# Kernel tuning notes

Hardware: AMD Instinct MI355X
Metric: run time of the kernel (lower is better)

## Reference

```python
import jax, jax.numpy as jnp
import numpy as np
import math

B, L, D, H = 4, 2048, 512, 8
DH = D // H
FACTOR = 5.0
EPS = 1e-9
# static top-k count: min(L_q, max(1, int(factor * log(L_q + eps))))
K_TOP = min(L, max(1, int(FACTOR * math.log(L + EPS))))  # = 38
SCALE = 1.0 / math.sqrt(DH)


def setup_inputs() -> dict:
    key = jax.random.key(0)
    ks = jax.random.split(key, 9)
    s = 1.0 / math.sqrt(D)
    return {
        "x": jax.random.normal(ks[0], (B, L, D), jnp.float32),
        "Wq": jax.random.normal(ks[1], (D, D), jnp.float32) * s,
        "bq": jax.random.normal(ks[2], (D,), jnp.float32) * 0.01,
        "Wk": jax.random.normal(ks[3], (D, D), jnp.float32) * s,
        "bk": jax.random.normal(ks[4], (D,), jnp.float32) * 0.01,
        "Wv": jax.random.normal(ks[5], (D, D), jnp.float32) * s,
        "bv": jax.random.normal(ks[6], (D,), jnp.float32) * 0.01,
        "Wo": jax.random.normal(ks[7], (D, D), jnp.float32) * s,
        "bo": jax.random.normal(ks[8], (D,), jnp.float32) * 0.01,
    }


def _project(x, W, b):
    # [B, L, D] -> [B*H, L, DH]
    y = x @ W + b
    return y.reshape(B, L, H, DH).transpose(0, 2, 1, 3).reshape(B * H, L, DH)


def reference(x, Wq, bq, Wk, bk, Wv, bv, Wo, bo):
    Q = _project(x, Wq, bq)
    K = _project(x, Wk, bk)
    V = _project(x, Wv, bv)

    # full scores for sparsity measure: [BH, L, L]
    scores = jnp.einsum('bqd,bkd->bqk', Q, K) * SCALE
    M = scores.max(axis=-1) - scores.mean(axis=-1)  # [BH, L]
    _, top_idx = jax.lax.top_k(M, K_TOP)            # [BH, K_TOP]

    # gather sparse queries, sparse attention
    Q_sparse = jnp.take_along_axis(Q, top_idx[:, :, None], axis=1)  # [BH, K_TOP, DH]
    scores_sparse = jnp.einsum('bqd,bkd->bqk', Q_sparse, K) * SCALE
    attn = jax.nn.softmax(scores_sparse, axis=-1)
    context_sparse = attn @ V                                        # [BH, K_TOP, DH]

    # mean-filled context, scatter sparse results back
    V_mean = V.mean(axis=1, keepdims=True)                           # [BH, 1, DH]
    context = jnp.broadcast_to(V_mean, (B * H, L, DH))
    bidx = jnp.arange(B * H)[:, None]
    context = context.at[bidx, top_idx, :].set(context_sparse)

    # merge heads, output projection
    out = context.reshape(B, H, L, DH).transpose(0, 2, 1, 3).reshape(B, L, D)
    return out @ Wo + bo
```

## Files before the change

### kernel.cpp

```cpp
#include <hip/hip_runtime.h>

#define BB   4
#define LL   2048
#define DD   512
#define HH   8
#define DH   64
#define BH   32
#define KTOP 38
#define NCAND 64
#define SCALEF 0.125f

#define NSP  16
#define CHK  128
#define QPAD 48
#define SCS  132
#define VST  66

typedef __attribute__((ext_vector_type(8))) short bf16x8;
typedef __attribute__((ext_vector_type(8))) unsigned short ushort8;
typedef __attribute__((ext_vector_type(4))) float f32x4;

__device__ __forceinline__ ushort f32_to_bf16_rn(float x) {
    unsigned u = __float_as_uint(x);
    u += 0x7fffu + ((u >> 16) & 1u);
    return (ushort)(u >> 16);
}
__device__ __forceinline__ float bf16_to_f32(ushort h) {
    return __uint_as_float(((unsigned)h) << 16);
}
__device__ __forceinline__ unsigned int pack_hl(float x) {
    ushort h = f32_to_bf16_rn(x);
    ushort l = f32_to_bf16_rn(x - bf16_to_f32(h));
    return ((unsigned int)l << 16) | (unsigned int)h;
}

__global__ __launch_bounds__(256) void split_x(const float* __restrict__ X,
                                               ushort* __restrict__ XH,
                                               ushort* __restrict__ XL) {
    const size_t c = (size_t)blockIdx.x * 256 + threadIdx.x;
    const float4 v = *(const float4*)&X[c * 4];
    ushort4 h, l;
    h.x = f32_to_bf16_rn(v.x); l.x = f32_to_bf16_rn(v.x - bf16_to_f32(h.x));
    h.y = f32_to_bf16_rn(v.y); l.y = f32_to_bf16_rn(v.y - bf16_to_f32(h.y));
    h.z = f32_to_bf16_rn(v.z); l.z = f32_to_bf16_rn(v.z - bf16_to_f32(h.z));
    h.w = f32_to_bf16_rn(v.w); l.w = f32_to_bf16_rn(v.w - bf16_to_f32(h.w));
    *(ushort4*)&XH[c * 4] = h;
    *(ushort4*)&XL[c * 4] = l;
}

__global__ __launch_bounds__(256) void split_wT(const float* __restrict__ W0,
                                                const float* __restrict__ W1,
                                                const float* __restrict__ W2,
                                                ushort* __restrict__ WTH,
                                                ushort* __restrict__ WTL) {
    __shared__ float tile[32][33];
    const int z = blockIdx.z;
    const float* W = (z == 0) ? W0 : (z == 1) ? W1 : W2;
    ushort* oh = WTH + (size_t)z * DD * DD;
    ushort* ol = WTL + (size_t)z * DD * DD;
    const int n0 = blockIdx.x * 32, k0 = blockIdx.y * 32;
    const int t = threadIdx.x;
    const int r = t >> 5, c = t & 31;
    #pragma unroll
    for (int i = 0; i < 4; i++)
        tile[r + i * 8][c] = W[(size_t)(k0 + r + i * 8) * DD + n0 + c];
    __syncthreads();
    #pragma unroll
    for (int i = 0; i < 4; i++) {
        int row = r + i * 8;
        float v = tile[c][row];
        ushort h = f32_to_bf16_rn(v);
        oh[(size_t)(n0 + row) * DD + k0 + c] = h;
        ol[(size_t)(n0 + row) * DD + k0 + c] = f32_to_bf16_rn(v - bf16_to_f32(h));
    }
}

__global__ __launch_bounds__(256) void mfma_gemm_qkv(const ushort* __restrict__ AH,
                                                     const ushort* __restrict__ AL,
                                                     const ushort* __restrict__ BTH,
                                                     const ushort* __restrict__ BTL,
                                                     const float* __restrict__ bq,
                                                     const float* __restrict__ bk,
                                                     const float* __restrict__ bv,
                                                     float* __restrict__ Qp,
                                                     float* __restrict__ Kp,
                                                     float* __restrict__ Vp,
                                                     ushort* __restrict__ KH) {
    __shared__ ushort BHs[64 * 72];
    __shared__ ushort BLs[64 * 72];

    const int t = threadIdx.x;
    const int w = t >> 6, lane = t & 63;
    const int quad = lane >> 4, n16 = lane & 15;
    const int row0 = blockIdx.y * 128;
    const int n0   = blockIdx.x * 64;
    const int z    = n0 >> 9;
    const int nloc0 = n0 & 511;

    const float* bias = (z == 0) ? bq : (z == 1) ? bk : bv;
    float* Y          = (z == 0) ? Qp : (z == 1) ? Kp : Vp;

    f32x4 acc[2][4] = {};

    size_t arow_off[2];
    #pragma unroll
    for (int mt = 0; mt < 2; mt++)
        arow_off[mt] = (size_t)(row0 + w * 32 + mt * 16 + n16) * DD;

    const size_t bbase = (size_t)z * DD * DD;

    for (int k0 = 0; k0 < DD; k0 += 64) {
        #pragma unroll
        for (int i = 0; i < 2; i++) {
            int s = i * 256 + t;
            int row = s >> 3, c8 = s & 7;
            const size_t goff = bbase + (size_t)(nloc0 + row) * DD + k0 + c8 * 8;
            *(uint4*)&BHs[row * 72 + c8 * 8] = *(const uint4*)&BTH[goff];
            *(uint4*)&BLs[row * 72 + c8 * 8] = *(const uint4*)&BTL[goff];
        }
        bf16x8 ah[2][2], al[2][2];
        #pragma unroll
        for (int mt = 0; mt < 2; mt++)
            #pragma unroll
            for (int kf = 0; kf < 2; kf++) {
                size_t off = arow_off[mt] + k0 + kf * 32 + quad * 8;
                ah[mt][kf] = *(const bf16x8*)&AH[off];
                al[mt][kf] = *(const bf16x8*)&AL[off];
            }
        __syncthreads();

        #pragma unroll
        for (int kf = 0; kf < 2; kf++)
            #pragma unroll
            for (int nt = 0; nt < 4; nt++) {
                int boff = (nt * 16 + n16) * 72 + kf * 32 + quad * 8;
                bf16x8 bh = *(const bf16x8*)&BHs[boff];
                bf16x8 bl = *(const bf16x8*)&BLs[boff];
                #pragma unroll
                for (int mt = 0; mt < 2; mt++) {
                    acc[mt][nt] = __builtin_amdgcn_mfma_f32_16x16x32_bf16(ah[mt][kf], bh, acc[mt][nt], 0, 0, 0);
                    acc[mt][nt] = __builtin_amdgcn_mfma_f32_16x16x32_bf16(ah[mt][kf], bl, acc[mt][nt], 0, 0, 0);
                    acc[mt][nt] = __builtin_amdgcn_mfma_f32_16x16x32_bf16(al[mt][kf], bh, acc[mt][nt], 0, 0, 0);
                }
            }
        __syncthreads();
    }

    #pragma unroll
    for (int mt = 0; mt < 2; mt++)
        #pragma unroll
        for (int nt = 0; nt < 4; nt++) {
            const int c = nloc0 + nt * 16 + n16;
            const float bvv = bias[c];
            const int h = c >> 6, dh = c & 63;
            #pragma unroll
            for (int r = 0; r < 4; r++) {
                int R = row0 + w * 32 + mt * 16 + quad * 4 + r;
                int b = R >> 11, l = R & 2047;
                float v = acc[mt][nt][r] + bvv;
                size_t off = (((size_t)(b * HH + h)) * LL + l) * DH + dh;
                Y[off] = v;
                if (z == 1) KH[off] = f32_to_bf16_rn(v);
            }
        }
}

__global__ __launch_bounds__(256) void mean_partial(const float* __restrict__ Kp,
                                                    const float* __restrict__ Vp,
                                                    float* __restrict__ partial) {
    __shared__ float red[256];
    const int bh = blockIdx.x;
    const int srcI = blockIdx.y;
    const int z  = blockIdx.z;
    const float* src = srcI ? Vp : Kp;
    const int t = threadIdx.x;
    const int d = t & 63, ch = t >> 6;
    const int l0 = z * 128 + ch * 32;
    float s = 0.f;
    for (int l = l0; l < l0 + 32; l++)
        s += src[((size_t)bh * LL + l) * DH + d];
    red[t] = s;
    __syncthreads();
    if (t < 64)
        partial[((size_t)((bh * 2 + srcI) * 16 + z)) * 64 + t] =
            red[t] + red[t + 64] + red[t + 128] + red[t + 192];
}

__global__ __launch_bounds__(64) void mean_reduce(const float* __restrict__ partial,
                                                  float* __restrict__ Kmean,
                                                  float* __restrict__ Vmean) {
    const int bh = blockIdx.x;
    const int srcI = blockIdx.y;
    const int t  = threadIdx.x;
    float s = 0.f;
    #pragma unroll
    for (int z = 0; z < 16; z++)
        s += partial[((size_t)((bh * 2 + srcI) * 16 + z)) * 64 + t];
    float* dst = srcI ? Vmean : Kmean;
    dst[bh * DH + t] = s * (1.0f / LL);
}

__global__ __launch_bounds__(256) void base_kernel(const float* __restrict__ Vmean,
                                                   const float* __restrict__ Wo,
                                                   const float* __restrict__ bo,
                                                   float* __restrict__ BASE) {
    __shared__ float vm[512];
    const int b = blockIdx.x;
    const int t = threadIdx.x;
    vm[t]       = Vmean[b * 512 + t];
    vm[t + 256] = Vmean[b * 512 + t + 256];
    __syncthreads();
    #pragma unroll
    for (int cc = 0; cc < 2; cc++) {
        const int c = cc * 256 + t;
        float s = 0.f;
        for (int k = 0; k < 512; k++) s += vm[k] * Wo[(size_t)k * 512 + c];
        BASE[b * 512 + c] = s + bo[c];
    }
}

__global__ __launch_bounds__(256) void broadcast_base(const float* __restrict__ BASE,
                                                      float* __restrict__ out) {
    const size_t f = ((size_t)blockIdx.x * 256 + threadIdx.x) * 4;
    const int b = (int)(f >> 20);
    const int c = (int)(f & 511);
    *(float4*)&out[f] = *(const float4*)&BASE[b * 512 + c];
}

__global__ __launch_bounds__(256) void scatter_kernel(const float* __restrict__ CORR,
                                                      const int* __restrict__ TIDX,
                                                      const float* __restrict__ Wo,
                                                      float* __restrict__ out) {
    __shared__ float cr[64];
    const int q = blockIdx.x, bh = blockIdx.y;
    const int b = bh >> 3, h = bh & 7;
    const int t = threadIdx.x;
    if (t < 64) cr[t] = CORR[((size_t)bh * KTOP + q) * DH + t];
    __syncthreads();
    const int l = TIDX[bh * KTOP + q];
    #pragma unroll
    for (int cc = 0; cc < 2; cc++) {
        const int c = cc * 256 + t;
        float s = 0.f;
        #pragma unroll
        for (int d = 0; d < 64; d++) s += cr[d] * Wo[(size_t)(h * 64 + d) * 512 + c];
        atomicAdd(&out[((size_t)b * LL + l) * DD + c], s);
    }
}

__global__ __launch_bounds__(256) void mfma_stats(const float* __restrict__ Qp,
                                                  const ushort* __restrict__ KH,
                                                  const float* __restrict__ Kmean,
                                                  float* __restrict__ MP,
                                                  float* __restrict__ MMD) {
    __shared__ ushort KS[128 * 72];
    __shared__ float  Km[64];

    const int bh = blockIdx.y;
    const int q0 = blockIdx.x * 128;
    const int z  = blockIdx.z;
    const int t    = threadIdx.x;
    const int w    = t >> 6;
    const int lane = t & 63;
    const int quad = lane >> 4;
    const int n16  = lane & 15;

    if (z == 0) {
        if (t < 64) Km[t] = Kmean[bh * DH + t];
        __syncthreads();
        if (t < 128) {
            const float4* qr = (const float4*)&Qp[((size_t)bh * LL + q0 + t) * DH];
            const float4* km4 = (const float4*)Km;
            float md = 0.f;
            #pragma unroll
            for (int i = 0; i < 16; i++) {
                float4 a = qr[i], b = km4[i];
                md += a.x * b.x + a.y * b.y + a.z * b.z + a.w * b.w;
            }
            MMD[(size_t)bh * LL + q0 + t] = SCALEF * md;
        }
    }

    bf16x8 aH[2][2], aL[2][2];
    #pragma unroll
    for (int mt = 0; mt < 2; mt++) {
        const float* qrp = &Qp[((size_t)bh * LL + q0 + w * 32 + mt * 16 + n16) * DH + quad * 8];
        float v[16];
        *(float4*)&v[0]  = *(const float4*)(qrp);
        *(float4*)&v[4]  = *(const float4*)(qrp + 4);
        *(float4*)&v[8]  = *(const float4*)(qrp + 32);
        *(float4*)&v[12] = *(const float4*)(qrp + 36);
        #pragma unroll
        for (int j = 0; j < 8; j++) {
            ushort h0 = f32_to_bf16_rn(v[j]);
            aH[mt][0][j] = (short)h0;
            aL[mt][0][j] = (short)f32_to_bf16_rn(v[j] - bf16_to_f32(h0));
            ushort h1 = f32_to_bf16_rn(v[8 + j]);
            aH[mt][1][j] = (short)h1;
            aL[mt][1][j] = (short)f32_to_bf16_rn(v[8 + j] - bf16_to_f32(h1));
        }
    }

    f32x4 maxv[2] = {{-3.4e38f, -3.4e38f, -3.4e38f, -3.4e38f},
                     {-3.4e38f, -3.4e38f, -3.4e38f, -3.4e38f}};

    const int kbase = z * (LL / 2);
    for (int kt0 = kbase; kt0 < kbase + LL / 2; kt0 += 128) {
        __syncthreads();
        #pragma unroll
        for (int i = 0; i < 4; i++) {
            int f = i * 256 + t;
            int row = f >> 3, c8 = f & 7;
            const uint4 v = *(const uint4*)&KH[((size_t)(bh * LL + kt0 + row)) * DH + c8 * 8];
            *(uint4*)&KS[row * 72 + c8 * 8] = v;
        }
        __syncthreads();

        for (int ktl = 0; ktl < 128; ktl += 16) {
            const ushort* bp = &KS[(size_t)(ktl + n16) * 72 + quad * 8];
            bf16x8 bH0 = *(const bf16x8*)(bp);
            bf16x8 bH1 = *(const bf16x8*)(bp + 32);
            #pragma unroll
            for (int mt = 0; mt < 2; mt++) {
                f32x4 acc = {0.f, 0.f, 0.f, 0.f};
                acc = __builtin_amdgcn_mfma_f32_16x16x32_bf16(aH[mt][0], bH0, acc, 0, 0, 0);
                acc = __builtin_amdgcn_mfma_f32_16x16x32_bf16(aH[mt][1], bH1, acc, 0, 0, 0);
                acc = __builtin_amdgcn_mfma_f32_16x16x32_bf16(aL[mt][0], bH0, acc, 0, 0, 0);
                acc = __builtin_amdgcn_mfma_f32_16x16x32_bf16(aL[mt][1], bH1, acc, 0, 0, 0);
                maxv[mt][0] = fmaxf(maxv[mt][0], acc[0]);
                maxv[mt][1] = fmaxf(maxv[mt][1], acc[1]);
                maxv[mt][2] = fmaxf(maxv[mt][2], acc[2]);
                maxv[mt][3] = fmaxf(maxv[mt][3], acc[3]);
            }
        }
    }

    #pragma unroll
    for (int off = 1; off < 16; off <<= 1)
        #pragma unroll
        for (int mt = 0; mt < 2; mt++)
            #pragma unroll
            for (int r = 0; r < 4; r++)
                maxv[mt][r] = fmaxf(maxv[mt][r], __shfl_xor(maxv[mt][r], off));

    if (n16 == 0) {
        #pragma unroll
        for (int mt = 0; mt < 2; mt++)
            #pragma unroll
            for (int r = 0; r < 4; r++) {
                int lq = w * 32 + mt * 16 + quad * 4 + r;
                MP[((size_t)z * BH + bh) * LL + q0 + lq] = SCALEF * maxv[mt][r];
            }
    }
}

__global__ __launch_bounds__(256) void topk_radix(const float* __restrict__ MP,
                                                  const float* __restrict__ MMD,
                                                  int* __restrict__ out_idx) {
    __shared__ unsigned hist[4096];
    __shared__ unsigned segc[256];
    __shared__ unsigned suf[256];
    __shared__ int sb1, sc1, sb2;
    __shared__ int ncnt;
    const int bh = blockIdx.x;
    const int t  = threadIdx.x;

    unsigned key[8];
    #pragma unroll
    for (int i = 0; i < 8; i++) {
        size_t q = (size_t)i * 256 + t;
        float v = fmaxf(MP[(size_t)bh * LL + q], MP[((size_t)BH + bh) * LL + q])
                  - MMD[(size_t)bh * LL + q];
        unsigned u = __float_as_uint(v);
        key[i] = (u & 0x80000000u) ? ~u : (u | 0x80000000u);
    }

    #pragma unroll
    for (int i = 0; i < 16; i++) hist[t * 16 + i] = 0;
    if (t == 0) ncnt = 0;
    __syncthreads();
    #pragma unroll
    for (int i = 0; i < 8; i++) atomicAdd(&hist[key[i] >> 20], 1u);
    __syncthreads();
    unsigned s = 0;
    #pragma unroll
    for (int i = 0; i < 16; i++) s += hist[t * 16 + i];
    segc[t] = s;
    __syncthreads();
    if (t == 0) {
        unsigned run = 0;
        for (int i = 255; i >= 0; i--) { suf[i] = run; run += segc[i]; }
    }
    __syncthreads();
    if (suf[t] < NCAND && suf[t] + segc[t] >= NCAND) {
        unsigned c = suf[t];
        for (int j = 15; j >= 0; j--) {
            int b = t * 16 + j;
            if (c + hist[b] >= NCAND) { sb1 = b; sc1 = (int)c; break; }
            c += hist[b];
        }
    }
    __syncthreads();
    const unsigned b1 = (unsigned)sb1;
    const int c1 = sc1;

    #pragma unroll
    for (int i = 0; i < 16; i++) hist[t * 16 + i] = 0;
    __syncthreads();
    #pragma unroll
    for (int i = 0; i < 8; i++)
        if ((key[i] >> 20) == b1) atomicAdd(&hist[(key[i] >> 8) & 0xfffu], 1u);
    __syncthreads();
    s = 0;
    #pragma unroll
    for (int i = 0; i < 16; i++) s += hist[t * 16 + i];
    segc[t] = s;
    __syncthreads();
    if (t == 0) {
        unsigned run = 0;
        for (int i = 255; i >= 0; i--) { suf[i] = run; run += segc[i]; }
    }
    __syncthreads();
    const int need2 = NCAND - c1;
    if ((int)suf[t] < need2 && (int)(suf[t] + segc[t]) >= need2) {
        unsigned c = suf[t];
        for (int j = 15; j >= 0; j--) {
            int b = t * 16 + j;
            if ((int)(c + hist[b]) >= need2) { sb2 = b; break; }
            c += hist[b];
        }
    }
    __syncthreads();
    const unsigned b2 = (unsigned)sb2;

    #pragma unroll
    for (int i = 0; i < 8; i++)
        if ((key[i] >> 20) > b1) {
            int p = atomicAdd(&ncnt, 1);
            out_idx[bh * NCAND + p] = i * 256 + t;
        }
    __syncthreads();
    #pragma unroll
    for (int i = 0; i < 8; i++)
        if ((key[i] >> 20) == b1 && ((key[i] >> 8) & 0xfffu) > b2) {
            int p = atomicAdd(&ncnt, 1);
            out_idx[bh * NCAND + p] = i * 256 + t;
        }
    __syncthreads();
    #pragma unroll
    for (int i = 0; i < 8; i++)
        if ((key[i] >> 20) == b1 && ((key[i] >> 8) & 0xfffu) == b2) {
            int p = atomicAdd(&ncnt, 1);
            if (p < NCAND) out_idx[bh * NCAND + p] = i * 256 + t;
        }
}

__global__ __launch_bounds__(256) void exact_partial(const float* __restrict__ Qp,
                                                     const float* __restrict__ Kp,
                                                     const int* __restrict__ CAND,
                                                     float* __restrict__ EMP) {
    __shared__ float Qs[64][65];
    __shared__ float Ks[64][65];
    __shared__ int   cidx[64];
    const int bh = blockIdx.y;
    const int chunk = blockIdx.x;
    const int t = threadIdx.x;
    const int tx = t & 15, ty = t >> 4;

    if (t < 64) cidx[t] = CAND[bh * NCAND + t];
    __syncthreads();
    #pragma unroll
    for (int i = 0; i < 4; i++) {
        int f = i * 256 + t;
        int row = f >> 4, c4 = f & 15;
        const float4 v = *(const float4*)&Qp[((size_t)bh * LL + cidx[row]) * DH + c4 * 4];
        *(float4*)&Qs[row][c4 * 4] = v;
    }

    float mx[4] = {-3.4e38f, -3.4e38f, -3.4e38f, -3.4e38f};

    for (int kt = 0; kt < 4; kt++) {
        __syncthreads();
        #pragma unroll
        for (int i = 0; i < 4; i++) {
            int f = i * 256 + t;
            int row = f >> 4, c4 = f & 15;
            const float4 v = *(const float4*)&Kp[((size_t)(bh * LL + chunk * 256 + kt * 64 + row)) * DH + c4 * 4];
            *(float4*)&Ks[row][c4 * 4] = v;
        }
        __syncthreads();
        float acc[4][4] = {};
        #pragma unroll 8
        for (int dd = 0; dd < 64; dd++) {
            float a[4], b[4];
            #pragma unroll
            for (int i = 0; i < 4; i++) a[i] = Qs[ty * 4 + i][dd];
            #pragma unroll
            for (int j = 0; j < 4; j++) b[j] = Ks[tx * 4 + j][dd];
            #pragma unroll
            for (int i = 0; i < 4; i++)
                #pragma unroll
                for (int j = 0; j < 4; j++) acc[i][j] += a[i] * b[j];
        }
        #pragma unroll
        for (int i = 0; i < 4; i++)
            #pragma unroll
            for (int j = 0; j < 4; j++) mx[i] = fmaxf(mx[i], acc[i][j]);
    }

    #pragma unroll
    for (int off = 1; off < 16; off <<= 1)
        #pragma unroll
        for (int i = 0; i < 4; i++)
            mx[i] = fmaxf(mx[i], __shfl_xor(mx[i], off));

    if (tx == 0) {
        #pragma unroll
        for (int i = 0; i < 4; i++)
            EMP[((size_t)bh * NCAND + ty * 4 + i) * 8 + chunk] = mx[i];
    }
}

__global__ __launch_bounds__(64) void select_kernel(const float* __restrict__ EMP,
                                                    const int* __restrict__ CAND,
                                                    const float* __restrict__ Qp,
                                                    const float* __restrict__ Kmean,
                                                    int* __restrict__ TIDX) {
    __shared__ float Km[64];
    const int bh = blockIdx.x;
    const int t  = threadIdx.x;
    Km[t] = Kmean[bh * DH + t];
    __syncthreads();

    const int qi = CAND[bh * NCAND + t];
    float mx = -3.4e38f;
    #pragma unroll
    for (int c = 0; c < 8; c++) mx = fmaxf(mx, EMP[((size_t)bh * NCAND + t) * 8 + c]);

    const float4* qr = (const float4*)&Qp[((size_t)bh * LL + qi) * DH];
    const float4* km4 = (const float4*)Km;
    float md = 0.f;
    #pragma unroll
    for (int i = 0; i < 16; i++) {
        float4 a = qr[i], b = km4[i];
        md += a.x * b.x + a.y * b.y + a.z * b.z + a.w * b.w;
    }
    float v = SCALEF * mx - SCALEF * md;

    for (int it = 0; it < KTOP; it++) {
        float bv = v; int bq = qi;
        #pragma unroll
        for (int off = 1; off < 64; off <<= 1) {
            float ov = __shfl_xor(bv, off);
            int   oq = __shfl_xor(bq, off);
            if (ov > bv || (ov == bv && oq < bq)) { bv = ov; bq = oq; }
        }
        if (t == 0) TIDX[bh * KTOP + it] = bq;
        if (qi == bq) v = -3.4e38f;
    }
}

__global__ __launch_bounds__(256) void sparse_partial(const float* __restrict__ Qp,
                                                      const ushort* __restrict__ KH,
                                                      const float* __restrict__ Vp,
                                                      const int* __restrict__ TIDX,
                                                      float* __restrict__ OPART,
                                                      float* __restrict__ MPART,
                                                      float* __restrict__ LPART) {
    __shared__ float sc[QPAD * SCS];
    __shared__ unsigned int Vhl[CHK * VST];
    const int bh = blockIdx.y;
    const int ck = blockIdx.x;
    const int k0 = ck * CHK;
    const int t = threadIdx.x;
    const int w = t >> 6, lane = t & 63;
    const int quad = lane >> 4, n16 = lane & 15;
    const int mt = w;

    #pragma unroll
    for (int i = 0; i < 8; i++) {
        int e = i * 256 + t;
        int key = e >> 4, c4 = e & 15;
        const float4 v = *(const float4*)&Vp[((size_t)(bh * LL + k0 + key)) * DH + c4 * 4];
        uint4 p;
        p.x = pack_hl(v.x); p.y = pack_hl(v.y);
        p.z = pack_hl(v.z); p.w = pack_hl(v.w);
        *(uint4*)&Vhl[key * VST + c4 * 4] = p;
    }

    if (mt < 3) {
        bf16x8 aH[2], aL[2];
        {
            int q = mt * 16 + n16;
            int qq = q < KTOP ? q : (KTOP - 1);
            const float* qp = &Qp[((size_t)bh * LL + TIDX[bh * KTOP + qq]) * DH];
            #pragma unroll
            for (int kf = 0; kf < 2; kf++) {
                float v[8];
                *(float4*)&v[0] = *(const float4*)(qp + kf * 32 + quad * 8);
                *(float4*)&v[4] = *(const float4*)(qp + kf * 32 + quad * 8 + 4);
                #pragma unroll
                for (int j = 0; j < 8; j++) {
                    ushort h = f32_to_bf16_rn(v[j]);
                    aH[kf][j] = (short)h;
                    aL[kf][j] = (short)f32_to_bf16_rn(v[j] - bf16_to_f32(h));
                }
            }
        }
        #pragma unroll
        for (int nt = 0; nt < 8; nt++) {
            f32x4 acc = {0.f, 0.f, 0.f, 0.f};
            #pragma unroll
            for (int kf = 0; kf < 2; kf++) {
                bf16x8 b = *(const bf16x8*)&KH[((size_t)(bh * LL + k0 + nt * 16 + n16)) * DH + kf * 32 + quad * 8];
                acc = __builtin_amdgcn_mfma_f32_16x16x32_bf16(aH[kf], b, acc, 0, 0, 0);
                acc = __builtin_amdgcn_mfma_f32_16x16x32_bf16(aL[kf], b, acc, 0, 0, 0);
            }
            #pragma unroll
            for (int r = 0; r < 4; r++)
                sc[(mt * 16 + quad * 4 + r) * SCS + nt * 16 + n16] = acc[r];
        }
    }
    __syncthreads();

    for (int row = w; row < KTOP; row += 4) {
        float v0 = sc[row * SCS + lane];
        float v1 = sc[row * SCS + 64 + lane];
        float m = fmaxf(v0, v1);
        #pragma unroll
        for (int off = 1; off < 64; off <<= 1)
            m = fmaxf(m, __shfl_xor(m, off));
        const float ms = m * SCALEF;
        float e0 = __expf(v0 * SCALEF - ms);
        float e1 = __expf(v1 * SCALEF - ms);
        float l = e0 + e1;
        #pragma unroll
        for (int off = 1; off < 64; off <<= 1)
            l += __shfl_xor(l, off);
        sc[row * SCS + lane]      = e0;
        sc[row * SCS + 64 + lane] = e1;
        if (lane == 0) {
            MPART[((size_t)ck * BH + bh) * KTOP + row] = ms;
            LPART[((size_t)ck * BH + bh) * KTOP + row] = l;
        }
    }
    __syncthreads();

    if (mt < 3) {
        f32x4 acc[4] = {};
        #pragma unroll
        for (int kf = 0; kf < 4; kf++) {
            bf16x8 ph, pl;
            {
                const float* pp = &sc[(mt * 16 + n16) * SCS + kf * 32 + quad * 8];
                float v[8];
                *(float4*)&v[0] = *(const float4*)(pp);
                *(float4*)&v[4] = *(const float4*)(pp + 4);
                #pragma unroll
                for (int j = 0; j < 8; j++) {
                    ushort h = f32_to_bf16_rn(v[j]);
                    ph[j] = (short)h;
                    pl[j] = (short)f32_to_bf16_rn(v[j] - bf16_to_f32(h));
                }
            }
            #pragma unroll
            for (int nt = 0; nt < 4; nt++) {
                unsigned int u[8];
                #pragma unroll
                for (int j = 0; j < 8; j++)
                    u[j] = Vhl[(kf * 32 + quad * 8 + j) * VST + nt * 16 + n16];
                bf16x8 vh, vl;
                #pragma unroll
                for (int j = 0; j < 8; j++) {
                    vh[j] = (short)(u[j] & 0xffffu);
                    vl[j] = (short)(u[j] >> 16);
                }
                acc[nt] = __builtin_amdgcn_mfma_f32_16x16x32_bf16(ph, vh, acc[nt], 0, 0, 0);
                acc[nt] = __builtin_amdgcn_mfma_f32_16x16x32_bf16(ph, vl, acc[nt], 0, 0, 0);
                acc[nt] = __builtin_amdgcn_mfma_f32_16x16x32_bf16(pl, vh, acc[nt], 0, 0, 0);
            }
        }
        #pragma unroll
        for (int nt = 0; nt < 4; nt++)
            #pragma unroll
            for (int r = 0; r < 4; r++) {
                int q = mt * 16 + quad * 4 + r;
                if (q < KTOP)
                    OPART[(((size_t)ck * BH + bh) * KTOP + q) * DH + nt * 16 + n16] = acc[nt][r];
            }
    }
}

__global__ __launch_bounds__(256) void sparse_combine(const float* __restrict__ OPART,
                                                      const float* __restrict__ MPART,
                                                      const float* __restrict__ LPART,
                                                      const float* __restrict__ Vmean,
                                                      float* __restrict__ CORR) {
    __shared__ float wts[NSP][KTOP];
    __shared__ float inv[KTOP];
    const int bh = blockIdx.x;
    const int t  = threadIdx.x;
    if (t < KTOP) {
        float m[NSP];
        float mx = -3.4e38f;
        #pragma unroll
        for (int c = 0; c < NSP; c++) {
            m[c] = MPART[((size_t)c * BH + bh) * KTOP + t];
            mx = fmaxf(mx, m[c]);
        }
        float L = 0.f;
        #pragma unroll
        for (int c = 0; c < NSP; c++) {
            float wc = __expf(m[c] - mx);
            wts[c][t] = wc;
            L += wc * LPART[((size_t)c * BH + bh) * KTOP + t];
        }
        inv[t] = 1.0f / L;
    }
    __syncthreads();
    for (int i = 0; i < 10; i++) {
        int idx = i * 256 + t;
        if (idx >= KTOP * DH) break;
        int q = idx >> 6, d = idx & 63;
        float o = 0.f;
        #pragma unroll
        for (int c = 0; c < NSP; c++)
            o += wts[c][q] * OPART[(((size_t)c * BH + bh) * KTOP + q) * DH + d];
        CORR[((size_t)bh * KTOP + q) * DH + d] = o * inv[q] - Vmean[bh * DH + d];
    }
}

extern "C" void kernel_launch(void* const* d_in, const int* in_sizes, int n_in,
                              void* d_out, int out_size, void* d_ws, size_t ws_size,
                              hipStream_t stream) {
    const float* x  = (const float*)d_in[0];
    const float* Wq = (const float*)d_in[1];
    const float* bq = (const float*)d_in[2];
    const float* Wk = (const float*)d_in[3];
    const float* bk = (const float*)d_in[4];
    const float* Wv = (const float*)d_in[5];
    const float* bv = (const float*)d_in[6];
    const float* Wo = (const float*)d_in[7];
    const float* bo = (const float*)d_in[8];
    float* out = (float*)d_out;

    float* ws = (float*)d_ws;
    const size_t QSZ = (size_t)BH * LL * DH;
    float* Qp    = ws;
    float* Kp    = ws + QSZ;
    float* Vp    = ws + 2 * QSZ;
    float* MMD   = ws + 3 * QSZ;
    float* KMEAN = MMD + (size_t)BH * LL;
    float* VMEAN = KMEAN + BH * DH;
    int*   CAND  = (int*)(VMEAN + BH * DH);
    int*   TIDX  = CAND + BH * NCAND;
    float* EMP   = (float*)(TIDX + BH * KTOP);
    float* MEANP = EMP + (size_t)BH * NCAND * 8;
    float* MP    = MEANP + 65536;
    float* CORR  = MP + (size_t)2 * BH * LL;
    float* BASE  = CORR + (size_t)BH * KTOP * DH;
    ushort* WTH  = (ushort*)(ws + 3 * QSZ + 786432);
    ushort* WTL  = WTH + (size_t)3 * DD * DD;
    ushort* XH   = WTL + (size_t)3 * DD * DD;
    ushort* XL   = XH + QSZ;
    ushort* KH   = XL + QSZ;
    float* OPART = (float*)(KH + QSZ);
    float* MPART = OPART + (size_t)NSP * BH * KTOP * DH;
    float* LPART = MPART + (size_t)NSP * BH * KTOP;

    split_wT<<<dim3(16, 16, 3), 256, 0, stream>>>(Wq, Wk, Wv, WTH, WTL);
    split_x<<<(int)(QSZ / 1024), 256, 0, stream>>>(x, XH, XL);

    mfma_gemm_qkv<<<dim3(24, 64), 256, 0, stream>>>(XH, XL, WTH, WTL,
                                                    bq, bk, bv, Qp, Kp, Vp, KH);

    mean_partial<<<dim3(BH, 2, 16), 256, 0, stream>>>(Kp, Vp, MEANP);
    mean_reduce<<<dim3(BH, 2), 64, 0, stream>>>(MEANP, KMEAN, VMEAN);

    base_kernel<<<BB, 256, 0, stream>>>(VMEAN, Wo, bo, BASE);
    broadcast_base<<<(int)(QSZ / 1024), 256, 0, stream>>>(BASE, out);

    mfma_stats<<<dim3(16, BH, 2), 256, 0, stream>>>(Qp, KH, KMEAN, MP, MMD);

    topk_radix<<<BH, 256, 0, stream>>>(MP, MMD, CAND);

    exact_partial<<<dim3(8, BH), 256, 0, stream>>>(Qp, Kp, CAND, EMP);

    select_kernel<<<BH, 64, 0, stream>>>(EMP, CAND, Qp, KMEAN, TIDX);

    sparse_partial<<<dim3(NSP, BH), 256, 0, stream>>>(Qp, KH, Vp, TIDX, OPART, MPART, LPART);
    sparse_combine<<<BH, 256, 0, stream>>>(OPART, MPART, LPART, VMEAN, CORR);

    scatter_kernel<<<dim3(KTOP, BH), 256, 0, stream>>>(CORR, TIDX, Wo, out);
}
```

Before: 312.1 us.

## Register-prefetch next tiles in QKV GEMM and stats; fold combine into scatter

The QKV projection GEMM and the stats kernel now prefetch the next k-tile (weights, activations, or K rows) into registers while MFMAs run on the current LDS tile. This hides global-load latency behind compute, at the cost of extra registers. The separate sparse_combine kernel is removed and its softmax-partial merge runs inside scatter_kernel. That saves one launch and the CORR round trip through memory, but each scatter block now recomputes the merge for its own query.

```diff
diff --git a/kernel.cpp b/kernel.cpp
--- a/kernel.cpp
+++ b/kernel.cpp
@@ -108,26 +108,54 @@
         arow_off[mt] = (size_t)(row0 + w * 32 + mt * 16 + n16) * DD;
 
     const size_t bbase = (size_t)z * DD * DD;
-
-    for (int k0 = 0; k0 < DD; k0 += 64) {
+    const int srow = t >> 3, sc8 = t & 7;
+
+    uint4 bregH[2], bregL[2];
+    #pragma unroll
+    for (int i = 0; i < 2; i++) {
+        const int row = srow + i * 32;
+        const size_t goff = bbase + (size_t)(nloc0 + row) * DD + sc8 * 8;
+        bregH[i] = *(const uint4*)&BTH[goff];
+        bregL[i] = *(const uint4*)&BTL[goff];
+    }
+    bf16x8 ah[2][2][2], al[2][2][2];
+    #pragma unroll
+    for (int mt = 0; mt < 2; mt++)
+        #pragma unroll
+        for (int kf = 0; kf < 2; kf++) {
+            size_t off = arow_off[mt] + kf * 32 + quad * 8;
+            ah[0][mt][kf] = *(const bf16x8*)&AH[off];
+            al[0][mt][kf] = *(const bf16x8*)&AL[off];
+        }
+
+    for (int k = 0; k < 8; k++) {
+        const int cur = k & 1, nxt = cur ^ 1;
         #pragma unroll
         for (int i = 0; i < 2; i++) {
-            int s = i * 256 + t;
-            int row = s >> 3, c8 = s & 7;
-            const size_t goff = bbase + (size_t)(nloc0 + row) * DD + k0 + c8 * 8;
-            *(uint4*)&BHs[row * 72 + c8 * 8] = *(const uint4*)&BTH[goff];
-            *(uint4*)&BLs[row * 72 + c8 * 8] = *(const uint4*)&BTL[goff];
-        }
-        bf16x8 ah[2][2], al[2][2];
-        #pragma unroll
-        for (int mt = 0; mt < 2; mt++)
-            #pragma unroll
-            for (int kf = 0; kf < 2; kf++) {
-                size_t off = arow_off[mt] + k0 + kf * 32 + quad * 8;
-                ah[mt][kf] = *(const bf16x8*)&AH[off];
-                al[mt][kf] = *(const bf16x8*)&AL[off];
-            }
+            const int row = srow + i * 32;
+            *(uint4*)&BHs[row * 72 + sc8 * 8] = bregH[i];
+            *(uint4*)&BLs[row * 72 + sc8 * 8] = bregL[i];
+        }
         __syncthreads();
+
+        if (k < 7) {
+            const int kn = (k + 1) * 64;
+            #pragma unroll
+            for (int i = 0; i < 2; i++) {
+                const int row = srow + i * 32;
+                const size_t goff = bbase + (size_t)(nloc0 + row) * DD + kn + sc8 * 8;
+                bregH[i] = *(const uint4*)&BTH[goff];
+                bregL[i] = *(const uint4*)&BTL[goff];
+            }
+            #pragma unroll
+            for (int mt = 0; mt < 2; mt++)
+                #pragma unroll
+                for (int kf = 0; kf < 2; kf++) {
+                    size_t off = arow_off[mt] + kn + kf * 32 + quad * 8;
+                    ah[nxt][mt][kf] = *(const bf16x8*)&AH[off];
+                    al[nxt][mt][kf] = *(const bf16x8*)&AL[off];
+                }
+        }
 
         #pragma unroll
         for (int kf = 0; kf < 2; kf++)
@@ -138,9 +166,9 @@
                 bf16x8 bl = *(const bf16x8*)&BLs[boff];
                 #pragma unroll
                 for (int mt = 0; mt < 2; mt++) {
-                    acc[mt][nt] = __builtin_amdgcn_mfma_f32_16x16x32_bf16(ah[mt][kf], bh, acc[mt][nt], 0, 0, 0);
-                    acc[mt][nt] = __builtin_amdgcn_mfma_f32_16x16x32_bf16(ah[mt][kf], bl, acc[mt][nt], 0, 0, 0);
-                    acc[mt][nt] = __builtin_amdgcn_mfma_f32_16x16x32_bf16(al[mt][kf], bh, acc[mt][nt], 0, 0, 0);
+                    acc[mt][nt] = __builtin_amdgcn_mfma_f32_16x16x32_bf16(ah[cur][mt][kf], bh, acc[mt][nt], 0, 0, 0);
+                    acc[mt][nt] = __builtin_amdgcn_mfma_f32_16x16x32_bf16(ah[cur][mt][kf], bl, acc[mt][nt], 0, 0, 0);
+                    acc[mt][nt] = __builtin_amdgcn_mfma_f32_16x16x32_bf16(al[cur][mt][kf], bh, acc[mt][nt], 0, 0, 0);
                 }
             }
         __syncthreads();
@@ -227,7 +255,10 @@
     *(float4*)&out[f] = *(const float4*)&BASE[b * 512 + c];
 }
 
-__global__ __launch_bounds__(256) void scatter_kernel(const float* __restrict__ CORR,
+__global__ __launch_bounds__(256) void scatter_kernel(const float* __restrict__ OPART,
+                                                      const float* __restrict__ MPART,
+                                                      const float* __restrict__ LPART,
+                                                      const float* __restrict__ Vmean,
                                                       const int* __restrict__ TIDX,
                                                       const float* __restrict__ Wo,
                                                       float* __restrict__ out) {
@@ -235,7 +266,27 @@
     const int q = blockIdx.x, bh = blockIdx.y;
     const int b = bh >> 3, h = bh & 7;
     const int t = threadIdx.x;
-    if (t < 64) cr[t] = CORR[((size_t)bh * KTOP + q) * DH + t];
+    if (t < 64) {
+        float m[NSP];
+        float mx = -3.4e38f;
+        #pragma unroll
+        for (int c = 0; c < NSP; c++) {
+            m[c] = MPART[((size_t)c * BH + bh) * KTOP + q];
+            mx = fmaxf(mx, m[c]);
+        }
+        float L = 0.f;
+        #pragma unroll
+        for (int c = 0; c < NSP; c++) {
+            m[c] = __expf(m[c] - mx);
+            L += m[c] * LPART[((size_t)c * BH + bh) * KTOP + q];
+        }
+        const float inv = 1.0f / L;
+        float o = 0.f;
+        #pragma unroll
+        for (int c = 0; c < NSP; c++)
+            o += m[c] * OPART[(((size_t)c * BH + bh) * KTOP + q) * DH + t];
+        cr[t] = o * inv - Vmean[bh * DH + t];
+    }
     __syncthreads();
     const int l = TIDX[bh * KTOP + q];
     #pragma unroll
@@ -264,6 +315,15 @@
     const int lane = t & 63;
     const int quad = lane >> 4;
     const int n16  = lane & 15;
+    const int kbase = z * (LL / 2);
+    const int srow = t >> 3, sc8 = t & 7;
+
+    uint4 sreg[4];
+    #pragma unroll
+    for (int i = 0; i < 4; i++) {
+        const int row = srow + i * 32;
+        sreg[i] = *(const uint4*)&KH[((size_t)(bh * LL + kbase + row)) * DH + sc8 * 8];
+    }
 
     if (z == 0) {
         if (t < 64) Km[t] = Kmean[bh * DH + t];
@@ -304,17 +364,21 @@
     f32x4 maxv[2] = {{-3.4e38f, -3.4e38f, -3.4e38f, -3.4e38f},
                      {-3.4e38f, -3.4e38f, -3.4e38f, -3.4e38f}};
 
-    const int kbase = z * (LL / 2);
-    for (int kt0 = kbase; kt0 < kbase + LL / 2; kt0 += 128) {
+    for (int tile = 0; tile < 8; tile++) {
+        #pragma unroll
+        for (int i = 0; i < 4; i++) {
+            const int row = srow + i * 32;
+            *(uint4*)&KS[row * 72 + sc8 * 8] = sreg[i];
+        }
         __syncthreads();
-        #pragma unroll
-        for (int i = 0; i < 4; i++) {
-            int f = i * 256 + t;
-            int row = f >> 3, c8 = f & 7;
-            const uint4 v = *(const uint4*)&KH[((size_t)(bh * LL + kt0 + row)) * DH + c8 * 8];
-            *(uint4*)&KS[row * 72 + c8 * 8] = v;
-        }
-        __syncthreads();
+        if (tile < 7) {
+            const int kt0 = kbase + (tile + 1) * 128;
+            #pragma unroll
+            for (int i = 0; i < 4; i++) {
+                const int row = srow + i * 32;
+                sreg[i] = *(const uint4*)&KH[((size_t)(bh * LL + kt0 + row)) * DH + sc8 * 8];
+            }
+        }
 
         for (int ktl = 0; ktl < 128; ktl += 16) {
             const ushort* bp = &KS[(size_t)(ktl + n16) * 72 + quad * 8];
@@ -333,6 +397,7 @@
                 maxv[mt][3] = fmaxf(maxv[mt][3], acc[3]);
             }
         }
+        __syncthreads();
     }
 
     #pragma unroll
@@ -691,45 +756,6 @@
     }
 }
 
-__global__ __launch_bounds__(256) void sparse_combine(const float* __restrict__ OPART,
-                                                      const float* __restrict__ MPART,
-                                                      const float* __restrict__ LPART,
-                                                      const float* __restrict__ Vmean,
-                                                      float* __restrict__ CORR) {
-    __shared__ float wts[NSP][KTOP];
-    __shared__ float inv[KTOP];
-    const int bh = blockIdx.x;
-    const int t  = threadIdx.x;
-    if (t < KTOP) {
-        float m[NSP];
-        float mx = -3.4e38f;
-        #pragma unroll
-        for (int c = 0; c < NSP; c++) {
-            m[c] = MPART[((size_t)c * BH + bh) * KTOP + t];
-            mx = fmaxf(mx, m[c]);
-        }
-        float L = 0.f;
-        #pragma unroll
-        for (int c = 0; c < NSP; c++) {
-            float wc = __expf(m[c] - mx);
-            wts[c][t] = wc;
-            L += wc * LPART[((size_t)c * BH + bh) * KTOP + t];
-        }
-        inv[t] = 1.0f / L;
-    }
-    __syncthreads();
-    for (int i = 0; i < 10; i++) {
-        int idx = i * 256 + t;
-        if (idx >= KTOP * DH) break;
-        int q = idx >> 6, d = idx & 63;
-        float o = 0.f;
-        #pragma unroll
-        for (int c = 0; c < NSP; c++)
-            o += wts[c][q] * OPART[(((size_t)c * BH + bh) * KTOP + q) * DH + d];
-        CORR[((size_t)bh * KTOP + q) * DH + d] = o * inv[q] - Vmean[bh * DH + d];
-    }
-}
-
 extern "C" void kernel_launch(void* const* d_in, const int* in_sizes, int n_in,
                               void* d_out, int out_size, void* d_ws, size_t ws_size,
                               hipStream_t stream) {
@@ -757,8 +783,7 @@
     float* EMP   = (float*)(TIDX + BH * KTOP);
     float* MEANP = EMP + (size_t)BH * NCAND * 8;
     float* MP    = MEANP + 65536;
-    float* CORR  = MP + (size_t)2 * BH * LL;
-    float* BASE  = CORR + (size_t)BH * KTOP * DH;
+    float* BASE  = MP + (size_t)2 * BH * LL;
     ushort* WTH  = (ushort*)(ws + 3 * QSZ + 786432);
     ushort* WTL  = WTH + (size_t)3 * DD * DD;
     ushort* XH   = WTL + (size_t)3 * DD * DD;
@@ -789,7 +814,7 @@
     select_kernel<<<BH, 64, 0, stream>>>(EMP, CAND, Qp, KMEAN, TIDX);
 
     sparse_partial<<<dim3(NSP, BH), 256, 0, stream>>>(Qp, KH, Vp, TIDX, OPART, MPART, LPART);
-    sparse_combine<<<BH, 256, 0, stream>>>(OPART, MPART, LPART, VMEAN, CORR);
-
-    scatter_kernel<<<dim3(KTOP, BH), 256, 0, stream>>>(CORR, TIDX, Wo, out);
-}
+
+    scatter_kernel<<<dim3(KTOP, BH), 256, 0, stream>>>(OPART, MPART, LPART, VMEAN,
+                                                       TIDX, Wo, out);
+}
```

After: 360.3 us. 15.5% more time.
